# Optimization experiments

Hardware: AMD Instinct MI355X
Metric: run time of the kernel (lower is better)

Reference implementation:

```python
import jax, jax.numpy as jnp
import numpy as np

D_MODEL = 1024
D_STATE = 16
K = 4           # conv kernel size
EXPAND = 2
D_INNER = EXPAND * D_MODEL
DT_RANK = 64    # ceil(D_MODEL / 16)
EPS = 1e-5
BATCH, L = 2, 1024


def setup_inputs() -> dict:
    key = jax.random.key(0)
    ks = jax.random.split(key, 11)
    s = 0.02
    return {
        "hidden_states": jax.random.normal(ks[0], (BATCH, L, D_MODEL), jnp.float32),
        "norm_w": jnp.ones((D_MODEL,), jnp.float32),
        "W_in": jax.random.normal(ks[1], (D_MODEL, 2 * D_INNER), jnp.float32) * s,
        "conv_w": jax.random.normal(ks[2], (D_INNER, K), jnp.float32) * 0.1,
        "conv_b": jax.random.normal(ks[3], (D_INNER,), jnp.float32) * s,
        "W_x": jax.random.normal(ks[4], (D_INNER, DT_RANK + 2 * D_STATE), jnp.float32) * s,
        "W_dt": jax.random.normal(ks[5], (DT_RANK, D_INNER), jnp.float32) * s,
        "b_dt": jax.random.normal(ks[6], (D_INNER,), jnp.float32) * s,
        # A kept negative for scan stability (init choice; math identical)
        "A": -jnp.exp(jax.random.normal(ks[7], (D_INNER, D_STATE), jnp.float32) * 0.5),
        "D": jax.random.normal(ks[8], (D_INNER,), jnp.float32) * s,
        "W_out": jax.random.normal(ks[9], (D_INNER, D_MODEL), jnp.float32) * s,
    }


def reference(hidden_states, norm_w, W_in, conv_w, conv_b, W_x, W_dt, b_dt, A, D, W_out):
    x0 = hidden_states                                # [B, L, d_model]
    # RMSNorm
    h = x0 * jax.lax.rsqrt(jnp.mean(x0 * x0, axis=-1, keepdims=True) + EPS) * norm_w
    # in_proj -> (x, res)
    x, res = jnp.split(h @ W_in, 2, axis=-1)          # each [B, L, d_inner]
    Bsz, Lq, _ = x.shape
    # causal depthwise conv1d (padding K-1 on left, truncate to L)
    xp = jnp.pad(x, ((0, 0), (K - 1, 0), (0, 0)))
    xc = sum(xp[:, j:j + Lq, :] * conv_w[:, j] for j in range(K)) + conv_b
    x = jax.nn.silu(xc)
    # x_proj -> delta, B, C
    xdbl = x @ W_x
    dlt, Bm, Cm = jnp.split(xdbl, [DT_RANK, DT_RANK + D_STATE], axis=-1)
    delta = jax.nn.softplus(dlt @ W_dt + b_dt)        # [B, L, d_inner]
    # selective scan
    deltaA = jnp.exp(jnp.einsum('bld,dn->bldn', delta, A))        # [B,L,d_in,n]
    dbu = (delta * x)[..., None] * Bm[:, :, None, :]              # [B,L,d_in,n]

    def step(carry, inp):
        dA, db, c = inp
        carry = dA * carry + db                       # [B, d_in, n]
        y = jnp.einsum('bdn,bn->bd', carry, c)
        return carry, y

    init = jnp.zeros((Bsz, D_INNER, D_STATE), x.dtype)
    _, ys = jax.lax.scan(step, init,
                         (deltaA.transpose(1, 0, 2, 3),
                          dbu.transpose(1, 0, 2, 3),
                          Cm.transpose(1, 0, 2)))
    y = ys.transpose(1, 0, 2) + x * D                 # [B, L, d_inner]
    y = y * jax.nn.silu(res)
    return x0 + y @ W_out
```

## Files before the change

kernel.cpp:

```cpp
#include <hip/hip_runtime.h>
#include <hip/hip_bf16.h>
#include <math.h>

#define BATCH 2
#define LSEQ 1024
#define DMODEL 1024
#define DINNER 2048
#define DSTATE 16
#define DTRANK 64
#define NROWS (BATCH * LSEQ)
#define XROW 128
#define NC 32
#define TCH (LSEQ / NC)

typedef __bf16 bf16;
typedef __attribute__((ext_vector_type(8))) __bf16 bf16x8;
typedef __attribute__((ext_vector_type(4))) float floatx4;

template<int MODE, bool BF16OUT, int TN_, int BK_>
__global__ __launch_bounds__(256) void gemm_bf16_kernel(
    const bf16* __restrict__ A, int lda,
    const bf16* __restrict__ Bt, int ldb,
    void* __restrict__ Cv, int ldc,
    int Ksplit,
    const float* __restrict__ bias,
    const float* __restrict__ resid, int ldr)
{
    constexpr int TMc  = 128;
    constexpr int CA   = BK_ / 8;
    constexpr int ISSA = TMc * BK_ * 2 / 4096;
    constexpr int ISSB = TN_ * BK_ * 2 / 4096;
    constexpr int NB   = TN_ / 32;
    constexpr int NH   = BK_ / 32;

    __shared__ __attribute__((aligned(16))) bf16 As[TMc * BK_];
    __shared__ __attribute__((aligned(16))) bf16 Bs[TN_ * BK_];

    const int tid  = threadIdx.x;
    const int lane = tid & 63;
    const int wave = tid >> 6;
    const int l15  = lane & 15;
    const int quad = lane >> 4;
    const int wm   = (wave >> 1) * 64;
    const int wn   = (wave & 1) * (TN_ / 2);

    const int row0 = blockIdx.y * TMc;
    const int col0 = blockIdx.x * TN_;
    const long kbase = (long)blockIdx.z * Ksplit;

    const bf16* gA[ISSA]; bf16* lA[ISSA];
    const bf16* gB[ISSB]; bf16* lB[ISSB];
    #pragma unroll
    for (int i = 0; i < ISSA; ++i) {
        int c = i * 256 + wave * 64 + lane;
        int r = c / CA;
        int kc = (c % CA) ^ (r % CA);
        gA[i] = A + (size_t)(row0 + r) * lda + kbase + kc * 8;
        lA[i] = As + (size_t)(i * 256 + wave * 64) * 8;
    }
    #pragma unroll
    for (int i = 0; i < ISSB; ++i) {
        int c = i * 256 + wave * 64 + lane;
        int r = c / CA;
        int kc = (c % CA) ^ (r % CA);
        gB[i] = Bt + (size_t)(col0 + r) * ldb + kbase + kc * 8;
        lB[i] = Bs + (size_t)(i * 256 + wave * 64) * 8;
    }

    floatx4 acc[4][NB];
    #pragma unroll
    for (int i = 0; i < 4; ++i)
        #pragma unroll
        for (int j = 0; j < NB; ++j)
            acc[i][j] = (floatx4){0.f, 0.f, 0.f, 0.f};

    const int kiters = Ksplit / BK_;
    for (int kk = 0; kk < kiters; ++kk) {
        __syncthreads();
        #pragma unroll
        for (int i = 0; i < ISSA; ++i) {
            __builtin_amdgcn_global_load_lds(
                (const __attribute__((address_space(1))) void*)gA[i],
                (__attribute__((address_space(3))) void*)lA[i], 16, 0, 0);
            gA[i] += BK_;
        }
        #pragma unroll
        for (int i = 0; i < ISSB; ++i) {
            __builtin_amdgcn_global_load_lds(
                (const __attribute__((address_space(1))) void*)gB[i],
                (__attribute__((address_space(3))) void*)lB[i], 16, 0, 0);
            gB[i] += BK_;
        }
        __syncthreads();

        #pragma unroll
        for (int h = 0; h < NH; ++h) {
            bf16x8 af[4], bfr[NB];
            #pragma unroll
            for (int i = 0; i < 4; ++i) {
                int r = wm + i * 16 + l15;
                af[i] = *(const bf16x8*)&As[(size_t)r * BK_ +
                          (((h * 4 + quad) ^ (r % CA)) * 8)];
            }
            #pragma unroll
            for (int j = 0; j < NB; ++j) {
                int r = wn + j * 16 + l15;
                bfr[j] = *(const bf16x8*)&Bs[(size_t)r * BK_ +
                           (((h * 4 + quad) ^ (r % CA)) * 8)];
            }
            #pragma unroll
            for (int i = 0; i < 4; ++i)
                #pragma unroll
                for (int j = 0; j < NB; ++j)
                    acc[i][j] = __builtin_amdgcn_mfma_f32_16x16x32_bf16(
                                    af[i], bfr[j], acc[i][j], 0, 0, 0);
        }
    }

    #pragma unroll
    for (int i = 0; i < 4; ++i) {
        #pragma unroll
        for (int j = 0; j < NB; ++j) {
            const int gn = col0 + wn + j * 16 + l15;
            #pragma unroll
            for (int r = 0; r < 4; ++r) {
                const int gm = row0 + wm + i * 16 + quad * 4 + r;
                float v = acc[i][j][r];
                if (MODE == 1) {
                    v += bias[gn];
                    v = (v > 20.0f) ? v : log1pf(__expf(v));
                }
                if (MODE == 2) v += resid[(size_t)gm * ldr + gn];
                if (MODE == 4) {
                    ((float*)Cv)[(size_t)blockIdx.z * ldr + (size_t)gm * ldc + gn] = v;
                } else if (BF16OUT) {
                    ((bf16*)Cv)[(size_t)gm * ldc + gn] = (bf16)v;
                } else {
                    ((float*)Cv)[(size_t)gm * ldc + gn] = v;
                }
            }
        }
    }
}

__global__ __launch_bounds__(256) void transpose_bf16_kernel(
    const float* __restrict__ W, bf16* __restrict__ Wt,
    int K, int N, int Npad)
{
    __shared__ float tile[32][33];
    const int n0 = blockIdx.x * 32;
    const int k0 = blockIdx.y * 32;
    const int tx = threadIdx.x & 31;
    const int ty = threadIdx.x >> 5;
    #pragma unroll
    for (int i = 0; i < 32; i += 8) {
        int k = k0 + ty + i, n = n0 + tx;
        tile[ty + i][tx] = (k < K && n < N) ? W[(size_t)k * N + n] : 0.0f;
    }
    __syncthreads();
    #pragma unroll
    for (int i = 0; i < 32; i += 8) {
        int n = n0 + ty + i, k = k0 + tx;
        if (n < Npad && k < K)
            Wt[(size_t)n * K + k] = (bf16)tile[tx][ty + i];
    }
}

__global__ __launch_bounds__(256) void rmsnorm_kernel(
    const float* __restrict__ x, const float* __restrict__ w,
    bf16* __restrict__ h)
{
    int row = blockIdx.x;
    int tid = threadIdx.x;
    const float* xr = x + (size_t)row * DMODEL;
    float4 v = *(const float4*)(xr + tid * 4);
    float ss = v.x * v.x + v.y * v.y + v.z * v.z + v.w * v.w;
    #pragma unroll
    for (int m = 32; m >= 1; m >>= 1) ss += __shfl_xor(ss, m);
    __shared__ float ws[4];
    if ((tid & 63) == 0) ws[tid >> 6] = ss;
    __syncthreads();
    float total = ws[0] + ws[1] + ws[2] + ws[3];
    float scale = rsqrtf(total * (1.0f / DMODEL) + 1e-5f);
    float4 wv = *(const float4*)(w + tid * 4);
    union { bf16 b[4]; uint2 u; } pk;
    pk.b[0] = (bf16)(v.x * scale * wv.x);
    pk.b[1] = (bf16)(v.y * scale * wv.y);
    pk.b[2] = (bf16)(v.z * scale * wv.z);
    pk.b[3] = (bf16)(v.w * scale * wv.w);
    *(uint2*)(h + (size_t)row * DMODEL + tid * 4) = pk.u;
}

__global__ __launch_bounds__(256) void conv_silu_kernel(
    const bf16* __restrict__ xz, const float* __restrict__ conv_w,
    const float* __restrict__ conv_b, bf16* __restrict__ xc)
{
    int idx = blockIdx.x * 256 + threadIdx.x;
    int c = idx & (DINNER - 1);
    int row = idx >> 11;
    int l = row & (LSEQ - 1);
    float w0 = conv_w[c * 4 + 0];
    float w1 = conv_w[c * 4 + 1];
    float w2 = conv_w[c * 4 + 2];
    float w3 = conv_w[c * 4 + 3];
    const bf16* xr = xz + (size_t)row * (2 * DINNER) + c;
    float acc = conv_b[c] + (float)xr[0] * w3;
    if (l >= 1) acc += (float)xr[-1 * 2 * DINNER] * w2;
    if (l >= 2) acc += (float)xr[-2 * 2 * DINNER] * w1;
    if (l >= 3) acc += (float)xr[-3 * 2 * DINNER] * w0;
    float s = acc / (1.0f + __expf(-acc));
    xc[idx] = (bf16)s;
}

__global__ __launch_bounds__(256) void xproj_reduce_kernel(
    const float* __restrict__ Pw, bf16* __restrict__ dt,
    float* __restrict__ BC)
{
    int idx = blockIdx.x * 256 + threadIdx.x;
    int row = idx >> 7, c = idx & 127;
    float s = 0.0f;
    #pragma unroll
    for (int k = 0; k < 8; ++k)
        s += Pw[(size_t)k * NROWS * XROW + idx];
    if (c < 64) dt[(size_t)row * 64 + c] = (bf16)s;
    else if (c < 96) BC[(size_t)row * 32 + (c - 64)] = s;
}

template<bool FINAL>
__global__ __launch_bounds__(256) void scan_chunk_kernel(
    const float* __restrict__ delta,
    const bf16* __restrict__ xc,
    const float* __restrict__ BC,
    const float* __restrict__ A,
    float* __restrict__ Pbuf,
    float* __restrict__ Sbuf,
    const bf16* __restrict__ xz,
    const float* __restrict__ Dp,
    bf16* __restrict__ ybf)
{
    __shared__ float sBC[TCH][32];
    const int tid   = threadIdx.x;
    const int chunk = blockIdx.x;
    const int d     = blockIdx.y * 256 + tid;
    const int b     = blockIdx.z;
    const int row0  = b * LSEQ + chunk * TCH;

    {
        int t = tid >> 3, c4 = (tid & 7) * 4;
        *(float4*)&sBC[t][c4] = *(const float4*)&BC[(size_t)(row0 + t) * 32 + c4];
    }

    float Ad[16];
    #pragma unroll
    for (int j = 0; j < 4; ++j) {
        float4 av = *(const float4*)&A[(size_t)d * DSTATE + j * 4];
        Ad[j*4+0] = av.x; Ad[j*4+1] = av.y; Ad[j*4+2] = av.z; Ad[j*4+3] = av.w;
    }

    const size_t psoff = ((size_t)(b * NC + chunk) * DINNER + d) * DSTATE;
    float S[16], P[16];
    if (FINAL) {
        #pragma unroll
        for (int j = 0; j < 4; ++j) {
            float4 sv = *(const float4*)&Sbuf[psoff + j * 4];
            S[j*4+0] = sv.x; S[j*4+1] = sv.y; S[j*4+2] = sv.z; S[j*4+3] = sv.w;
        }
    } else {
        #pragma unroll
        for (int n = 0; n < 16; ++n) { S[n] = 0.0f; P[n] = 1.0f; }
    }
    float Dpd = FINAL ? Dp[d] : 0.0f;

    __syncthreads();

    #pragma unroll 2
    for (int t = 0; t < TCH; ++t) {
        const size_t row = (size_t)(row0 + t);
        float dv = delta[row * DINNER + d];
        float xv = (float)xc[row * DINNER + d];
        float u  = dv * xv;
        float yp[4] = {0.f, 0.f, 0.f, 0.f};
        #pragma unroll
        for (int n = 0; n < 16; ++n) {
            float dA = __expf(dv * Ad[n]);
            S[n] = dA * S[n] + u * sBC[t][n];
            if (FINAL) {
                yp[n & 3] += S[n] * sBC[t][16 + n];
            } else {
                P[n] *= dA;
            }
        }
        if (FINAL) {
            float y = (yp[0] + yp[1]) + (yp[2] + yp[3]);
            float res = (float)xz[row * (2 * DINNER) + DINNER + d];
            float sres = res / (1.0f + __expf(-res));
            ybf[row * DINNER + d] = (bf16)((y + xv * Dpd) * sres);
        }
    }

    if (!FINAL) {
        #pragma unroll
        for (int j = 0; j < 4; ++j) {
            *(float4*)&Pbuf[psoff + j * 4] =
                (float4){P[j*4+0], P[j*4+1], P[j*4+2], P[j*4+3]};
            *(float4*)&Sbuf[psoff + j * 4] =
                (float4){S[j*4+0], S[j*4+1], S[j*4+2], S[j*4+3]};
        }
    }
}

__global__ __launch_bounds__(256) void scan_combine_kernel(
    const float* __restrict__ Pbuf, float* __restrict__ Sbuf)
{
    int gid = blockIdx.x * 256 + threadIdx.x;
    int b = gid >> 15;
    int dn = gid & 32767;
    float carry = 0.0f;
    for (int k = 0; k < NC; ++k) {
        size_t off = ((size_t)(b * NC + k) << 15) + dn;
        float pk = Pbuf[off];
        float sk = Sbuf[off];
        Sbuf[off] = carry;
        carry = pk * carry + sk;
    }
}

extern "C" void kernel_launch(void* const* d_in, const int* in_sizes, int n_in,
                              void* d_out, int out_size, void* d_ws, size_t ws_size,
                              hipStream_t stream)
{
    const float* x0     = (const float*)d_in[0];
    const float* norm_w = (const float*)d_in[1];
    const float* W_in   = (const float*)d_in[2];
    const float* conv_w = (const float*)d_in[3];
    const float* conv_b = (const float*)d_in[4];
    const float* W_x    = (const float*)d_in[5];
    const float* W_dt   = (const float*)d_in[6];
    const float* b_dt   = (const float*)d_in[7];
    const float* A      = (const float*)d_in[8];
    const float* Dp     = (const float*)d_in[9];
    const float* W_out  = (const float*)d_in[10];
    float* out = (float*)d_out;

    char* p = (char*)d_ws;
    bf16*  xz_bf = (bf16*)p;            p += (size_t)NROWS * 2 * DINNER * 2;
    float* Pw    = (float*)p;           p += (size_t)8 * NROWS * XROW * 4;
    float* BC    = (float*)p;           p += (size_t)NROWS * 32 * 4;
    float* delta = (float*)p;           p += (size_t)NROWS * DINNER * 4;
    float* Pbuf  = (float*)p;           p += (size_t)BATCH * NC * DINNER * 16 * 4;
    float* Sbuf  = (float*)p;           p += (size_t)BATCH * NC * DINNER * 16 * 4;
    bf16*  h_bf  = (bf16*)p;            p += (size_t)NROWS * DMODEL * 2;
    bf16*  xc_bf = (bf16*)p;            p += (size_t)NROWS * DINNER * 2;
    bf16*  y_bf  = (bf16*)p;            p += (size_t)NROWS * DINNER * 2;
    bf16*  WinT  = (bf16*)p;            p += (size_t)(2*DINNER) * DMODEL * 2;
    bf16*  WxT   = (bf16*)p;            p += (size_t)XROW * DINNER * 2;
    bf16*  WdtT  = (bf16*)p;            p += (size_t)DINNER * DTRANK * 2;
    bf16*  WoutT = (bf16*)p;            p += (size_t)DMODEL * DINNER * 2;
    bf16*  dt_bf = (bf16*)p;            p += (size_t)NROWS * DTRANK * 2;

    transpose_bf16_kernel<<<dim3(128, 32), 256, 0, stream>>>(W_in,  WinT,  DMODEL, 2*DINNER, 2*DINNER);
    transpose_bf16_kernel<<<dim3(4, 64),   256, 0, stream>>>(W_x,   WxT,   DINNER, 96, XROW);
    transpose_bf16_kernel<<<dim3(64, 2),   256, 0, stream>>>(W_dt,  WdtT,  DTRANK, DINNER, DINNER);
    transpose_bf16_kernel<<<dim3(32, 64),  256, 0, stream>>>(W_out, WoutT, DINNER, DMODEL, DMODEL);

    rmsnorm_kernel<<<NROWS, 256, 0, stream>>>(x0, norm_w, h_bf);

    gemm_bf16_kernel<0, true, 128, 64><<<dim3(32, 16, 1), 256, 0, stream>>>(
        h_bf, DMODEL, WinT, DMODEL, xz_bf, 2*DINNER, DMODEL, nullptr, nullptr, 0);

    conv_silu_kernel<<<(NROWS * DINNER) / 256, 256, 0, stream>>>(xz_bf, conv_w, conv_b, xc_bf);

    gemm_bf16_kernel<4, false, 128, 64><<<dim3(1, 16, 8), 256, 0, stream>>>(
        xc_bf, DINNER, WxT, DINNER, Pw, XROW, DINNER / 8, nullptr, nullptr, NROWS * XROW);

    xproj_reduce_kernel<<<(NROWS * XROW) / 256, 256, 0, stream>>>(Pw, dt_bf, BC);

    gemm_bf16_kernel<1, false, 128, 64><<<dim3(16, 16, 1), 256, 0, stream>>>(
        dt_bf, DTRANK, WdtT, DTRANK, delta, DINNER, DTRANK, b_dt, nullptr, 0);

    dim3 sgrid(NC, DINNER / 256, BATCH);
    scan_chunk_kernel<false><<<sgrid, 256, 0, stream>>>(
        delta, xc_bf, BC, A, Pbuf, Sbuf, nullptr, nullptr, nullptr);
    scan_combine_kernel<<<(BATCH * DINNER * DSTATE) / 256, 256, 0, stream>>>(Pbuf, Sbuf);
    scan_chunk_kernel<true><<<sgrid, 256, 0, stream>>>(
        delta, xc_bf, BC, A, Pbuf, Sbuf, xz_bf, Dp, y_bf);

    gemm_bf16_kernel<2, false, 64, 64><<<dim3(16, 16, 1), 256, 0, stream>>>(
        y_bf, DINNER, WoutT, DINNER, out, DMODEL, DINNER, nullptr, x0, DMODEL);
}
```

Before: 278.5 us.

## Fuse prep kernels, vectorize conv, store delta in bf16, coalesce scan state

Merges the four weight-transpose launches and RMSNorm into one prep kernel to cut launch overhead. The conv+SiLU kernel now handles two channels per thread with vector loads. Delta is written as bf16 instead of fp32, halving its traffic in the GEMM epilogue and both scan passes at some cost in precision. Scan chunk state P/S moves to an n-major layout so per-state stores and loads coalesce across d.

```diff
diff --git a/kernel.cpp b/kernel.cpp
--- a/kernel.cpp
+++ b/kernel.cpp
@@ -15,6 +15,7 @@
 
 typedef __bf16 bf16;
 typedef __attribute__((ext_vector_type(8))) __bf16 bf16x8;
+typedef __attribute__((ext_vector_type(2))) __bf16 bf16x2;
 typedef __attribute__((ext_vector_type(4))) float floatx4;
 
 template<int MODE, bool BF16OUT, int TN_, int BK_>
@@ -143,52 +144,58 @@
     }
 }
 
-__global__ __launch_bounds__(256) void transpose_bf16_kernel(
-    const float* __restrict__ W, bf16* __restrict__ Wt,
-    int K, int N, int Npad)
-{
-    __shared__ float tile[32][33];
-    const int n0 = blockIdx.x * 32;
-    const int k0 = blockIdx.y * 32;
-    const int tx = threadIdx.x & 31;
-    const int ty = threadIdx.x >> 5;
-    #pragma unroll
-    for (int i = 0; i < 32; i += 8) {
-        int k = k0 + ty + i, n = n0 + tx;
-        tile[ty + i][tx] = (k < K && n < N) ? W[(size_t)k * N + n] : 0.0f;
-    }
-    __syncthreads();
-    #pragma unroll
-    for (int i = 0; i < 32; i += 8) {
-        int n = n0 + ty + i, k = k0 + tx;
-        if (n < Npad && k < K)
-            Wt[(size_t)n * K + k] = (bf16)tile[tx][ty + i];
-    }
-}
-
-__global__ __launch_bounds__(256) void rmsnorm_kernel(
-    const float* __restrict__ x, const float* __restrict__ w,
+__global__ __launch_bounds__(256) void prep_kernel(
+    const float* __restrict__ W_in,  bf16* __restrict__ WinT,
+    const float* __restrict__ W_x,   bf16* __restrict__ WxT,
+    const float* __restrict__ W_dt,  bf16* __restrict__ WdtT,
+    const float* __restrict__ W_out, bf16* __restrict__ WoutT,
+    const float* __restrict__ x0, const float* __restrict__ norm_w,
     bf16* __restrict__ h)
 {
-    int row = blockIdx.x;
-    int tid = threadIdx.x;
-    const float* xr = x + (size_t)row * DMODEL;
-    float4 v = *(const float4*)(xr + tid * 4);
-    float ss = v.x * v.x + v.y * v.y + v.z * v.z + v.w * v.w;
-    #pragma unroll
-    for (int m = 32; m >= 1; m >>= 1) ss += __shfl_xor(ss, m);
-    __shared__ float ws[4];
-    if ((tid & 63) == 0) ws[tid >> 6] = ss;
-    __syncthreads();
-    float total = ws[0] + ws[1] + ws[2] + ws[3];
-    float scale = rsqrtf(total * (1.0f / DMODEL) + 1e-5f);
-    float4 wv = *(const float4*)(w + tid * 4);
-    union { bf16 b[4]; uint2 u; } pk;
-    pk.b[0] = (bf16)(v.x * scale * wv.x);
-    pk.b[1] = (bf16)(v.y * scale * wv.y);
-    pk.b[2] = (bf16)(v.z * scale * wv.z);
-    pk.b[3] = (bf16)(v.w * scale * wv.w);
-    *(uint2*)(h + (size_t)row * DMODEL + tid * 4) = pk.u;
+    __shared__ float smem[32 * 33];
+    const int bid = blockIdx.x;
+    const int tid = threadIdx.x;
+
+    if (bid < 6528) {
+        const float* W; bf16* Wt; int K, N, Npad, bx, by;
+        if (bid < 4096)      { W = W_in;  Wt = WinT;  K = 1024; N = 4096; Npad = 4096; bx = bid & 127, by = bid >> 7; }
+        else if (bid < 4352) { int l = bid - 4096; W = W_x;  Wt = WxT;  K = 2048; N = 96;   Npad = 128;  bx = l & 3,  by = l >> 2; }
+        else if (bid < 4480) { int l = bid - 4352; W = W_dt; Wt = WdtT; K = 64;   N = 2048; Npad = 2048; bx = l & 63, by = l >> 6; }
+        else                 { int l = bid - 4480; W = W_out;Wt = WoutT;K = 2048; N = 1024; Npad = 1024; bx = l & 31, by = l >> 5; }
+        float (*tile)[33] = (float(*)[33])smem;
+        const int n0 = bx * 32, k0 = by * 32;
+        const int tx = tid & 31, ty = tid >> 5;
+        #pragma unroll
+        for (int i = 0; i < 32; i += 8) {
+            int k = k0 + ty + i, n = n0 + tx;
+            tile[ty + i][tx] = (k < K && n < N) ? W[(size_t)k * N + n] : 0.0f;
+        }
+        __syncthreads();
+        #pragma unroll
+        for (int i = 0; i < 32; i += 8) {
+            int n = n0 + ty + i, k = k0 + tx;
+            if (n < Npad && k < K)
+                Wt[(size_t)n * K + k] = (bf16)tile[tx][ty + i];
+        }
+    } else {
+        const int row = bid - 6528;
+        const float* xr = x0 + (size_t)row * DMODEL;
+        float4 v = *(const float4*)(xr + tid * 4);
+        float ss = v.x * v.x + v.y * v.y + v.z * v.z + v.w * v.w;
+        #pragma unroll
+        for (int m = 32; m >= 1; m >>= 1) ss += __shfl_xor(ss, m);
+        if ((tid & 63) == 0) smem[tid >> 6] = ss;
+        __syncthreads();
+        float total = smem[0] + smem[1] + smem[2] + smem[3];
+        float scale = rsqrtf(total * (1.0f / DMODEL) + 1e-5f);
+        float4 wv = *(const float4*)(norm_w + tid * 4);
+        union { bf16 b[4]; uint2 u; } pk;
+        pk.b[0] = (bf16)(v.x * scale * wv.x);
+        pk.b[1] = (bf16)(v.y * scale * wv.y);
+        pk.b[2] = (bf16)(v.z * scale * wv.z);
+        pk.b[3] = (bf16)(v.w * scale * wv.w);
+        *(uint2*)(h + (size_t)row * DMODEL + tid * 4) = pk.u;
+    }
 }
 
 __global__ __launch_bounds__(256) void conv_silu_kernel(
@@ -196,20 +203,23 @@
     const float* __restrict__ conv_b, bf16* __restrict__ xc)
 {
     int idx = blockIdx.x * 256 + threadIdx.x;
-    int c = idx & (DINNER - 1);
-    int row = idx >> 11;
+    int c2 = (idx & (DINNER / 2 - 1)) * 2;
+    int row = idx >> 10;
     int l = row & (LSEQ - 1);
-    float w0 = conv_w[c * 4 + 0];
-    float w1 = conv_w[c * 4 + 1];
-    float w2 = conv_w[c * 4 + 2];
-    float w3 = conv_w[c * 4 + 3];
-    const bf16* xr = xz + (size_t)row * (2 * DINNER) + c;
-    float acc = conv_b[c] + (float)xr[0] * w3;
-    if (l >= 1) acc += (float)xr[-1 * 2 * DINNER] * w2;
-    if (l >= 2) acc += (float)xr[-2 * 2 * DINNER] * w1;
-    if (l >= 3) acc += (float)xr[-3 * 2 * DINNER] * w0;
-    float s = acc / (1.0f + __expf(-acc));
-    xc[idx] = (bf16)s;
+    float4 wA = *(const float4*)&conv_w[c2 * 4];
+    float4 wB = *(const float4*)&conv_w[c2 * 4 + 4];
+    float2 bb = *(const float2*)&conv_b[c2];
+    const bf16* xr = xz + (size_t)row * (2 * DINNER) + c2;
+    bf16x2 p0 = *(const bf16x2*)xr;
+    float a0 = bb.x + (float)p0[0] * wA.w;
+    float a1 = bb.y + (float)p0[1] * wB.w;
+    if (l >= 1) { bf16x2 p = *(const bf16x2*)(xr - 2 * DINNER); a0 += (float)p[0] * wA.z; a1 += (float)p[1] * wB.z; }
+    if (l >= 2) { bf16x2 p = *(const bf16x2*)(xr - 4 * DINNER); a0 += (float)p[0] * wA.y; a1 += (float)p[1] * wB.y; }
+    if (l >= 3) { bf16x2 p = *(const bf16x2*)(xr - 6 * DINNER); a0 += (float)p[0] * wA.x; a1 += (float)p[1] * wB.x; }
+    a0 = a0 / (1.0f + __expf(-a0));
+    a1 = a1 / (1.0f + __expf(-a1));
+    bf16x2 o; o[0] = (bf16)a0; o[1] = (bf16)a1;
+    *(bf16x2*)(xc + (size_t)row * DINNER + c2) = o;
 }
 
 __global__ __launch_bounds__(256) void xproj_reduce_kernel(
@@ -228,7 +238,7 @@
 
 template<bool FINAL>
 __global__ __launch_bounds__(256) void scan_chunk_kernel(
-    const float* __restrict__ delta,
+    const bf16* __restrict__ delta,
     const bf16* __restrict__ xc,
     const float* __restrict__ BC,
     const float* __restrict__ A,
@@ -257,14 +267,11 @@
         Ad[j*4+0] = av.x; Ad[j*4+1] = av.y; Ad[j*4+2] = av.z; Ad[j*4+3] = av.w;
     }
 
-    const size_t psoff = ((size_t)(b * NC + chunk) * DINNER + d) * DSTATE;
+    const size_t psbase = ((size_t)(b * NC + chunk) * DSTATE) * DINNER + d;
     float S[16], P[16];
     if (FINAL) {
         #pragma unroll
-        for (int j = 0; j < 4; ++j) {
-            float4 sv = *(const float4*)&Sbuf[psoff + j * 4];
-            S[j*4+0] = sv.x; S[j*4+1] = sv.y; S[j*4+2] = sv.z; S[j*4+3] = sv.w;
-        }
+        for (int n = 0; n < 16; ++n) S[n] = Sbuf[psbase + (size_t)n * DINNER];
     } else {
         #pragma unroll
         for (int n = 0; n < 16; ++n) { S[n] = 0.0f; P[n] = 1.0f; }
@@ -276,7 +283,7 @@
     #pragma unroll 2
     for (int t = 0; t < TCH; ++t) {
         const size_t row = (size_t)(row0 + t);
-        float dv = delta[row * DINNER + d];
+        float dv = (float)delta[row * DINNER + d];
         float xv = (float)xc[row * DINNER + d];
         float u  = dv * xv;
         float yp[4] = {0.f, 0.f, 0.f, 0.f};
@@ -300,11 +307,9 @@
 
     if (!FINAL) {
         #pragma unroll
-        for (int j = 0; j < 4; ++j) {
-            *(float4*)&Pbuf[psoff + j * 4] =
-                (float4){P[j*4+0], P[j*4+1], P[j*4+2], P[j*4+3]};
-            *(float4*)&Sbuf[psoff + j * 4] =
-                (float4){S[j*4+0], S[j*4+1], S[j*4+2], S[j*4+3]};
+        for (int n = 0; n < 16; ++n) {
+            Pbuf[psbase + (size_t)n * DINNER] = P[n];
+            Sbuf[psbase + (size_t)n * DINNER] = S[n];
         }
     }
 }
@@ -314,10 +319,10 @@
 {
     int gid = blockIdx.x * 256 + threadIdx.x;
     int b = gid >> 15;
-    int dn = gid & 32767;
+    int nd = gid & 32767;
     float carry = 0.0f;
     for (int k = 0; k < NC; ++k) {
-        size_t off = ((size_t)(b * NC + k) << 15) + dn;
+        size_t off = ((size_t)(b * NC + k) << 15) + nd;
         float pk = Pbuf[off];
         float sk = Sbuf[off];
         Sbuf[off] = carry;
@@ -346,7 +351,7 @@
     bf16*  xz_bf = (bf16*)p;            p += (size_t)NROWS * 2 * DINNER * 2;
     float* Pw    = (float*)p;           p += (size_t)8 * NROWS * XROW * 4;
     float* BC    = (float*)p;           p += (size_t)NROWS * 32 * 4;
-    float* delta = (float*)p;           p += (size_t)NROWS * DINNER * 4;
+    bf16*  delta = (bf16*)p;            p += (size_t)NROWS * DINNER * 2;
     float* Pbuf  = (float*)p;           p += (size_t)BATCH * NC * DINNER * 16 * 4;
     float* Sbuf  = (float*)p;           p += (size_t)BATCH * NC * DINNER * 16 * 4;
     bf16*  h_bf  = (bf16*)p;            p += (size_t)NROWS * DMODEL * 2;
@@ -358,24 +363,20 @@
     bf16*  WoutT = (bf16*)p;            p += (size_t)DMODEL * DINNER * 2;
     bf16*  dt_bf = (bf16*)p;            p += (size_t)NROWS * DTRANK * 2;
 
-    transpose_bf16_kernel<<<dim3(128, 32), 256, 0, stream>>>(W_in,  WinT,  DMODEL, 2*DINNER, 2*DINNER);
-    transpose_bf16_kernel<<<dim3(4, 64),   256, 0, stream>>>(W_x,   WxT,   DINNER, 96, XROW);
-    transpose_bf16_kernel<<<dim3(64, 2),   256, 0, stream>>>(W_dt,  WdtT,  DTRANK, DINNER, DINNER);
-    transpose_bf16_kernel<<<dim3(32, 64),  256, 0, stream>>>(W_out, WoutT, DINNER, DMODEL, DMODEL);
-
-    rmsnorm_kernel<<<NROWS, 256, 0, stream>>>(x0, norm_w, h_bf);
+    prep_kernel<<<8576, 256, 0, stream>>>(W_in, WinT, W_x, WxT, W_dt, WdtT,
+                                          W_out, WoutT, x0, norm_w, h_bf);
 
     gemm_bf16_kernel<0, true, 128, 64><<<dim3(32, 16, 1), 256, 0, stream>>>(
         h_bf, DMODEL, WinT, DMODEL, xz_bf, 2*DINNER, DMODEL, nullptr, nullptr, 0);
 
-    conv_silu_kernel<<<(NROWS * DINNER) / 256, 256, 0, stream>>>(xz_bf, conv_w, conv_b, xc_bf);
+    conv_silu_kernel<<<(NROWS * DINNER / 2) / 256, 256, 0, stream>>>(xz_bf, conv_w, conv_b, xc_bf);
 
     gemm_bf16_kernel<4, false, 128, 64><<<dim3(1, 16, 8), 256, 0, stream>>>(
         xc_bf, DINNER, WxT, DINNER, Pw, XROW, DINNER / 8, nullptr, nullptr, NROWS * XROW);
 
     xproj_reduce_kernel<<<(NROWS * XROW) / 256, 256, 0, stream>>>(Pw, dt_bf, BC);
 
-    gemm_bf16_kernel<1, false, 128, 64><<<dim3(16, 16, 1), 256, 0, stream>>>(
+    gemm_bf16_kernel<1, true, 128, 64><<<dim3(16, 16, 1), 256, 0, stream>>>(
         dt_bf, DTRANK, WdtT, DTRANK, delta, DINNER, DTRANK, b_dt, nullptr, 0);
 
     dim3 sgrid(NC, DINNER / 256, BATCH);
```

Measured after the change: 259.7 us. 6.7% less time.
